# Performance work log

Measured on AMD Instinct MI355X. Metric: run time of the kernel, lower is better.

## Reference

```python
import jax, jax.numpy as jnp
import numpy as np

B, S, D, H, F = 4, 2048, 1024, 16, 4096
BS = 64               # sparse attention block size
DH = D // H           # head dim
EPS = 1e-5


def _layer_norm(x, g, b):
    m = jnp.mean(x, axis=-1, keepdims=True)
    v = jnp.mean(jnp.square(x - m), axis=-1, keepdims=True)
    return (x - m) * jax.lax.rsqrt(v + EPS) * g + b


def setup_inputs() -> dict:
    key = jax.random.key(0)
    ks = jax.random.split(key, 12)
    sc = 0.02
    return {
        "hidden_states": jax.random.normal(ks[0], (B, S, D), dtype=jnp.float32),
        "ln1_g": jnp.ones((D,), jnp.float32), "ln1_b": jnp.zeros((D,), jnp.float32),
        "ln2_g": jnp.ones((D,), jnp.float32), "ln2_b": jnp.zeros((D,), jnp.float32),
        "wq": jax.random.normal(ks[1], (D, D), jnp.float32) * sc, "bq": jnp.zeros((D,), jnp.float32),
        "wk": jax.random.normal(ks[2], (D, D), jnp.float32) * sc, "bk": jnp.zeros((D,), jnp.float32),
        "wv": jax.random.normal(ks[3], (D, D), jnp.float32) * sc, "bv": jnp.zeros((D,), jnp.float32),
        "wo": jax.random.normal(ks[4], (D, D), jnp.float32) * sc, "bo": jnp.zeros((D,), jnp.float32),
        "w1": jax.random.normal(ks[5], (D, F), jnp.float32) * sc, "b1": jnp.zeros((F,), jnp.float32),
        "w2": jax.random.normal(ks[6], (F, D), jnp.float32) * sc, "b2": jnp.zeros((D,), jnp.float32),
    }


def _heads(x, w, b):
    # [B,S,D] -> [B,H,S/BS,BS,DH] block layout
    y = (x @ w + b).reshape(B, S, H, DH).transpose(0, 2, 1, 3)
    return y.reshape(B, H, S // BS, BS, DH)


def _block_attention(x, wq, bq, wk, bk, wv, bv, wo, bo):
    q = _heads(x, wq, bq)
    k = _heads(x, wk, bk)
    v = _heads(x, wv, bv)
    scores = jnp.einsum("bhnqd,bhnkd->bhnqk", q, k) / jnp.sqrt(jnp.float32(DH))
    w = jax.nn.softmax(scores, axis=-1)           # block-local (sparse) attention weights
    o = jnp.einsum("bhnqk,bhnkd->bhnqd", w, v)
    o = o.reshape(B, H, S, DH).transpose(0, 2, 1, 3).reshape(B, S, D)
    return o @ wo + bo, w


def reference(hidden_states, ln1_g, ln1_b, ln2_g, ln2_b,
              wq, bq, wk, bk, wv, bv, wo, bo, w1, b1, w2, b2):
    # pre-norm attention + residual
    x1 = _layer_norm(hidden_states, ln1_g, ln1_b)
    attn_out, attn_w = _block_attention(x1, wq, bq, wk, bk, wv, bv, wo, bo)
    h = hidden_states + attn_out
    # pre-norm FFN + residual (exact GELU, matching torch nn.GELU default)
    x2 = _layer_norm(h, ln2_g, ln2_b)
    ff = jax.nn.gelu(x2 @ w1 + b1, approximate=False) @ w2 + b2
    return h + ff, attn_w
```

## Files before the change

kernel.cpp:

```cpp
#include <hip/hip_runtime.h>
#include <hip/hip_bf16.h>
#include <cmath>

using bf16 = __hip_bfloat16;
typedef __attribute__((ext_vector_type(8))) short short8;
typedef __attribute__((ext_vector_type(4))) float f32x4;

#define LDK 72

__device__ __forceinline__ float bf2f(bf16 v){ return __bfloat162float(v); }
__device__ __forceinline__ bf16 f2bf(float v){ return __float2bfloat16(v); }

__device__ __forceinline__ void ld16(const void* g, void* l) {
    __builtin_amdgcn_global_load_lds(
        (const __attribute__((address_space(1))) void*)g,
        (__attribute__((address_space(3))) void*)l, 16, 0, 0);
}

__device__ __forceinline__ float gelu_f(float x) {
    float u = 0.7978845608028654f * x * (1.0f + 0.044715f * x * x);
    float e = __expf(2.0f * u);
    float t = 1.0f - 2.0f / (e + 1.0f);
    return 0.5f * x * (1.0f + t);
}

__global__ __launch_bounds__(256) void transpose_f32_bf16(
    const float* __restrict__ in, bf16* __restrict__ out, int R, int C)
{
    __shared__ __align__(16) bf16 tile[64][72];
    const int c0 = blockIdx.x * 64, r0 = blockIdx.y * 64;
    const int t = threadIdx.x;
    const int lr = t >> 3, lc = (t & 7) * 8;
    for (int p = 0; p < 2; ++p) {
        int r = p * 32 + lr;
        const float* src = in + (size_t)(r0 + r) * C + c0 + lc;
        float4 a = *(const float4*)src;
        float4 b = *(const float4*)(src + 4);
        tile[r][lc + 0] = f2bf(a.x); tile[r][lc + 1] = f2bf(a.y);
        tile[r][lc + 2] = f2bf(a.z); tile[r][lc + 3] = f2bf(a.w);
        tile[r][lc + 4] = f2bf(b.x); tile[r][lc + 5] = f2bf(b.y);
        tile[r][lc + 6] = f2bf(b.z); tile[r][lc + 7] = f2bf(b.w);
    }
    __syncthreads();
    for (int p = 0; p < 2; ++p) {
        int r = p * 32 + lr;
        short8 v;
        for (int j = 0; j < 8; ++j) v[j] = *(const short*)&tile[lc + j][r];
        *(short8*)(out + (size_t)(c0 + r) * R + r0 + lc) = v;
    }
}

__global__ __launch_bounds__(256) void concat_bias(
    const float* __restrict__ bq, const float* __restrict__ bk,
    const float* __restrict__ bv, float* __restrict__ out)
{
    int i = blockIdx.x * 256 + threadIdx.x;
    const float* src = (i < 1024) ? bq : ((i < 2048) ? bk : bv);
    out[i] = src[i & 1023];
}

__global__ __launch_bounds__(256) void layernorm_k(
    const float* __restrict__ x, const float* __restrict__ g,
    const float* __restrict__ bta, bf16* __restrict__ out)
{
    const int row = blockIdx.x, t = threadIdx.x;
    const float* xr = x + (size_t)row * 1024;
    float v[4], s1 = 0.f, s2 = 0.f;
    for (int j = 0; j < 4; ++j) {
        float f = xr[j * 256 + t];
        v[j] = f; s1 += f; s2 += f * f;
    }
    for (int d = 1; d < 64; d <<= 1) { s1 += __shfl_xor(s1, d); s2 += __shfl_xor(s2, d); }
    __shared__ float red[2][4];
    int wave = t >> 6, lane = t & 63;
    if (lane == 0) { red[0][wave] = s1; red[1][wave] = s2; }
    __syncthreads();
    s1 = red[0][0] + red[0][1] + red[0][2] + red[0][3];
    s2 = red[1][0] + red[1][1] + red[1][2] + red[1][3];
    float mean = s1 * (1.0f / 1024.0f);
    float var  = s2 * (1.0f / 1024.0f) - mean * mean;
    float rs   = rsqrtf(var + 1e-5f);
    bf16* orow = out + (size_t)row * 1024;
    for (int j = 0; j < 4; ++j) {
        int c = j * 256 + t;
        orow[c] = f2bf((v[j] - mean) * rs * g[c] + bta[c]);
    }
}

template <int MODE, int TM>
__global__ __launch_bounds__(256, (TM == 128 ? 3 : 4)) void gemm_bt(
    const bf16* __restrict__ A, const bf16* __restrict__ Bt,
    const float* __restrict__ bias, const float* __restrict__ res,
    void* __restrict__ C, int M, int N, int K)
{
    constexpr int MI = TM / 32;
    constexpr int AR = TM / 64;
    __shared__ __align__(16) bf16 As0[TM * 32];
    __shared__ __align__(16) bf16 Bs0[128 * 32];
    __shared__ __align__(16) bf16 As1[TM * 32];
    __shared__ __align__(16) bf16 Bs1[128 * 32];
    const int m0 = blockIdx.x * TM, n0 = blockIdx.y * 128;
    const int t = threadIdx.x;
    const int wave = t >> 6, lane = t & 63, lhi = lane >> 4, llo = lane & 15;
    const int wm = (wave & 1) * (TM / 2), wn = (wave >> 1) * 64;

    const int srow = t >> 2;
    const int sg   = (t & 3) ^ ((t >> 3) & 3);
    const bf16* Asrc = A  + (size_t)(m0 + srow) * K + sg * 8;
    const bf16* Bsrc = Bt + (size_t)(n0 + srow) * K + sg * 8;

    int offA[MI], offB[4];
    for (int i = 0; i < MI; ++i) {
        int row = wm + i * 16 + llo;
        offA[i] = row * 32 + (lhi ^ ((row >> 1) & 3)) * 8;
    }
    for (int i = 0; i < 4; ++i) {
        int row = wn + i * 16 + llo;
        offB[i] = row * 32 + (lhi ^ ((row >> 1) & 3)) * 8;
    }

    f32x4 acc[MI][4];
    for (int i = 0; i < MI; ++i)
        for (int j = 0; j < 4; ++j) acc[i][j] = (f32x4){0.f, 0.f, 0.f, 0.f};

    auto issue = [&](int k0, bf16* As, bf16* Bs) {
        for (int p = 0; p < AR; ++p)
            ld16(Asrc + (size_t)p * 64 * K + k0, As + p * 2048 + wave * 512);
        for (int p = 0; p < 2; ++p)
            ld16(Bsrc + (size_t)p * 64 * K + k0, Bs + p * 2048 + wave * 512);
    };
    auto compute = [&](const bf16* As, const bf16* Bs) {
        short8 af[MI], bfr[4];
        for (int i = 0; i < MI; ++i) af[i]  = *(const short8*)&As[offA[i]];
        for (int i = 0; i < 4;  ++i) bfr[i] = *(const short8*)&Bs[offB[i]];
        for (int mi = 0; mi < MI; ++mi)
            for (int ni = 0; ni < 4; ++ni)
                acc[mi][ni] = __builtin_amdgcn_mfma_f32_16x16x32_bf16(
                    af[mi], bfr[ni], acc[mi][ni], 0, 0, 0);
    };

    issue(0, As0, Bs0);
    for (int k0 = 0; k0 < K; k0 += 64) {
        __syncthreads();
        issue(k0 + 32, As1, Bs1);
        compute(As0, Bs0);
        __syncthreads();
        if (k0 + 64 < K) issue(k0 + 64, As0, Bs0);
        compute(As1, Bs1);
    }

    for (int mi = 0; mi < MI; ++mi)
        for (int ni = 0; ni < 4; ++ni) {
            int row = m0 + wm + mi * 16 + lhi * 4;
            int col = n0 + wn + ni * 16 + llo;
            float bcol = bias[col];
            size_t base = (size_t)row * N + col;
            for (int r = 0; r < 4; ++r) {
                size_t idx = base + (size_t)r * N;
                float v = acc[mi][ni][r] + bcol;
                if (MODE == 0) {
                    ((bf16*)C)[idx] = f2bf(v);
                } else if (MODE == 1) {
                    ((float*)C)[idx] = v + res[idx];
                } else if (MODE == 2) {
                    ((bf16*)C)[idx] = f2bf(gelu_f(v));
                } else {
                    ((float*)C)[idx] = v + res[idx];
                }
            }
        }
}

__global__ __launch_bounds__(256) void attn_kernel(
    const bf16* __restrict__ qkv, float* __restrict__ attw, bf16* __restrict__ o)
{
    __shared__ __align__(16) bf16 qs[64][LDK];
    __shared__ __align__(16) bf16 ks[64][LDK];
    __shared__ __align__(16) bf16 vs[64][LDK];
    const int gid = blockIdx.x;
    const int blk = gid & 31, h = (gid >> 5) & 15, b = gid >> 9;
    const int t = threadIdx.x, wave = t >> 6, lane = t & 63;
    const int lhi = lane >> 4, llo = lane & 15;
    const int srow = t >> 3, scol = (t & 7) * 8;

    for (int p = 0; p < 2; ++p) {
        int r = p * 32 + srow;
        const bf16* base = qkv + (size_t)(b * 2048 + blk * 64 + r) * 3072 + h * 64 + scol;
        *(short8*)&qs[r][scol] = *(const short8*)(base);
        *(short8*)&ks[r][scol] = *(const short8*)(base + 1024);
        *(short8*)&vs[r][scol] = *(const short8*)(base + 2048);
    }
    __syncthreads();

    f32x4 sacc[4];
    for (int j = 0; j < 4; ++j) sacc[j] = (f32x4){0.f, 0.f, 0.f, 0.f};
    for (int kk = 0; kk < 64; kk += 32) {
        short8 aq = *(const short8*)&qs[wave * 16 + llo][kk + lhi * 8];
        for (int j = 0; j < 4; ++j) {
            short8 bk = *(const short8*)&ks[j * 16 + llo][kk + lhi * 8];
            sacc[j] = __builtin_amdgcn_mfma_f32_16x16x32_bf16(aq, bk, sacc[j], 0, 0, 0);
        }
    }
    float inv[4];
    for (int r = 0; r < 4; ++r) {
        float m = -1e30f;
        for (int j = 0; j < 4; ++j) m = fmaxf(m, sacc[j][r]);
        for (int d = 1; d < 16; d <<= 1) m = fmaxf(m, __shfl_xor(m, d));
        float s = 0.f;
        for (int j = 0; j < 4; ++j) {
            float e = expf((sacc[j][r] - m) * 0.125f);
            sacc[j][r] = e; s += e;
        }
        for (int d = 1; d < 16; d <<= 1) s += __shfl_xor(s, d);
        inv[r] = 1.0f / s;
    }
    __syncthreads();
    const size_t wbase = (size_t)gid * 4096;
    for (int j = 0; j < 4; ++j)
        for (int r = 0; r < 4; ++r) {
            int row = wave * 16 + lhi * 4 + r, col = j * 16 + llo;
            float pw = sacc[j][r] * inv[r];
            qs[row][col] = f2bf(pw);
            attw[wbase + row * 64 + col] = pw;
        }
    __syncthreads();

    f32x4 oacc[4];
    for (int nt = 0; nt < 4; ++nt) oacc[nt] = (f32x4){0.f, 0.f, 0.f, 0.f};
    for (int kk = 0; kk < 64; kk += 32) {
        short8 aw = *(const short8*)&qs[wave * 16 + llo][kk + lhi * 8];
        for (int nt = 0; nt < 4; ++nt) {
            short8 bv;
            for (int jj = 0; jj < 8; ++jj)
                bv[jj] = *(const short*)&vs[kk + lhi * 8 + jj][nt * 16 + llo];
            oacc[nt] = __builtin_amdgcn_mfma_f32_16x16x32_bf16(aw, bv, oacc[nt], 0, 0, 0);
        }
    }
    for (int nt = 0; nt < 4; ++nt)
        for (int r = 0; r < 4; ++r) {
            int row = wave * 16 + lhi * 4 + r, col = nt * 16 + llo;
            o[(size_t)(b * 2048 + blk * 64 + row) * 1024 + h * 64 + col] = f2bf(oacc[nt][r]);
        }
}

extern "C" void kernel_launch(void* const* d_in, const int* in_sizes, int n_in,
                              void* d_out, int out_size, void* d_ws, size_t ws_size,
                              hipStream_t stream)
{
    const float* hidden = (const float*)d_in[0];
    const float* ln1_g  = (const float*)d_in[1];
    const float* ln1_b  = (const float*)d_in[2];
    const float* ln2_g  = (const float*)d_in[3];
    const float* ln2_b  = (const float*)d_in[4];
    const float* wq = (const float*)d_in[5];  const float* bq = (const float*)d_in[6];
    const float* wk = (const float*)d_in[7];  const float* bk = (const float*)d_in[8];
    const float* wv = (const float*)d_in[9];  const float* bv = (const float*)d_in[10];
    const float* wo = (const float*)d_in[11]; const float* bo = (const float*)d_in[12];
    const float* w1 = (const float*)d_in[13]; const float* b1 = (const float*)d_in[14];
    const float* w2 = (const float*)d_in[15]; const float* b2 = (const float*)d_in[16];

    char* ws = (char*)d_ws;
    const size_t MB = 1u << 20;
    bf16*  wqkvT   = (bf16*)(ws +  0 * MB);
    bf16*  woT     = (bf16*)(ws +  6 * MB);
    bf16*  w1T     = (bf16*)(ws +  8 * MB);
    bf16*  w2T     = (bf16*)(ws + 16 * MB);
    float* biasQKV = (float*)(ws + 24 * MB);
    bf16*  x       = (bf16*)(ws + 25 * MB);
    bf16*  qkv     = (bf16*)(ws + 41 * MB);
    float* hbuf    = (float*)(ws + 41 * MB);
    bf16*  ffc     = (bf16*)(ws + 73 * MB);
    bf16*  obuf    = (bf16*)(ws + 89 * MB);

    float* out0 = (float*)d_out;
    float* attw = (float*)d_out + (size_t)8192 * 1024;

    transpose_f32_bf16<<<dim3(16, 16), 256, 0, stream>>>(wq, wqkvT,                 1024, 1024);
    transpose_f32_bf16<<<dim3(16, 16), 256, 0, stream>>>(wk, wqkvT + 1024 * 1024,   1024, 1024);
    transpose_f32_bf16<<<dim3(16, 16), 256, 0, stream>>>(wv, wqkvT + 2*1024*1024,   1024, 1024);
    transpose_f32_bf16<<<dim3(16, 16), 256, 0, stream>>>(wo, woT, 1024, 1024);
    transpose_f32_bf16<<<dim3(64, 16), 256, 0, stream>>>(w1, w1T, 1024, 4096);
    transpose_f32_bf16<<<dim3(16, 64), 256, 0, stream>>>(w2, w2T, 4096, 1024);
    concat_bias<<<12, 256, 0, stream>>>(bq, bk, bv, biasQKV);

    layernorm_k<<<8192, 256, 0, stream>>>(hidden, ln1_g, ln1_b, x);

    gemm_bt<0, 128><<<dim3(64, 24), 256, 0, stream>>>(x, wqkvT, biasQKV, nullptr, qkv,
                                                      8192, 3072, 1024);

    attn_kernel<<<2048, 256, 0, stream>>>(qkv, attw, obuf);

    gemm_bt<1, 64><<<dim3(128, 8), 256, 0, stream>>>(obuf, woT, bo, hidden, hbuf,
                                                     8192, 1024, 1024);

    layernorm_k<<<8192, 256, 0, stream>>>(hbuf, ln2_g, ln2_b, x);

    gemm_bt<2, 128><<<dim3(64, 32), 256, 0, stream>>>(x, w1T, b1, nullptr, ffc,
                                                      8192, 4096, 1024);

    gemm_bt<3, 64><<<dim3(128, 8), 256, 0, stream>>>(ffc, w2T, b2, hbuf, out0,
                                                     8192, 1024, 4096);
}
```

Measured before the change: 484.2 us.

## Triple-buffer GEMM LDS tiles with one barrier per k-step

```diff
diff --git a/kernel.cpp b/kernel.cpp
--- a/kernel.cpp
+++ b/kernel.cpp
@@ -93,12 +93,11 @@
     const float* __restrict__ bias, const float* __restrict__ res,
     void* __restrict__ C, int M, int N, int K)
 {
-    constexpr int MI = TM / 32;
-    constexpr int AR = TM / 64;
-    __shared__ __align__(16) bf16 As0[TM * 32];
-    __shared__ __align__(16) bf16 Bs0[128 * 32];
-    __shared__ __align__(16) bf16 As1[TM * 32];
-    __shared__ __align__(16) bf16 Bs1[128 * 32];
+    constexpr int MI  = TM / 32;
+    constexpr int AR  = TM / 64;
+    constexpr int LPI = AR + 2;
+    __shared__ __align__(16) bf16 Asb[3][TM * 32];
+    __shared__ __align__(16) bf16 Bsb[3][128 * 32];
     const int m0 = blockIdx.x * TM, n0 = blockIdx.y * 128;
     const int t = threadIdx.x;
     const int wave = t >> 6, lane = t & 63, lhi = lane >> 4, llo = lane & 15;
@@ -123,11 +122,11 @@
     for (int i = 0; i < MI; ++i)
         for (int j = 0; j < 4; ++j) acc[i][j] = (f32x4){0.f, 0.f, 0.f, 0.f};
 
-    auto issue = [&](int k0, bf16* As, bf16* Bs) {
+    auto issue = [&](int k0, int b) {
         for (int p = 0; p < AR; ++p)
-            ld16(Asrc + (size_t)p * 64 * K + k0, As + p * 2048 + wave * 512);
+            ld16(Asrc + (size_t)p * 64 * K + k0, &Asb[b][p * 2048 + wave * 512]);
         for (int p = 0; p < 2; ++p)
-            ld16(Bsrc + (size_t)p * 64 * K + k0, Bs + p * 2048 + wave * 512);
+            ld16(Bsrc + (size_t)p * 64 * K + k0, &Bsb[b][p * 2048 + wave * 512]);
     };
     auto compute = [&](const bf16* As, const bf16* Bs) {
         short8 af[MI], bfr[4];
@@ -139,15 +138,17 @@
                     af[mi], bfr[ni], acc[mi][ni], 0, 0, 0);
     };
 
-    issue(0, As0, Bs0);
-    for (int k0 = 0; k0 < K; k0 += 64) {
-        __syncthreads();
-        issue(k0 + 32, As1, Bs1);
-        compute(As0, Bs0);
-        __syncthreads();
-        if (k0 + 64 < K) issue(k0 + 64, As0, Bs0);
-        compute(As1, Bs1);
-    }
+    const int S = K >> 5;
+    issue(0, 0);
+    issue(32, 1);
+    for (int i = 0; i < S; ++i) {
+        asm volatile("s_waitcnt vmcnt(%0) lgkmcnt(0)" :: "n"(LPI) : "memory");
+        __builtin_amdgcn_s_barrier();
+        int kp = i + 2 < S ? (i + 2) * 32 : 0;
+        issue(kp, (i + 2) % 3);
+        compute(Asb[i % 3], Bsb[i % 3]);
+    }
+    asm volatile("s_waitcnt vmcnt(0)" ::: "memory");
 
     for (int mi = 0; mi < MI; ++mi)
         for (int ni = 0; ni < 4; ++ni) {
```

New measurement: 492.1 us. About the same (+1.6%).
